# Optimization experiments

Hardware: AMD Instinct MI355X
Metric: run time of the kernel (lower is better)

## Reference

```python
import jax, jax.numpy as jnp
import numpy as np

B, H, W, C = 4, 128, 128, 256
SHIFTS_LOCAL = (1, 2, 4, 8)
SHIFTS_GLOBAL = (1, 2)
LN_EPS = 1e-6
BN_EPS = 1e-3
LAYER_SCALE_INIT = 1e-5


def _glorot(key, shape, fan_in, fan_out):
    lim = (6.0 / (fan_in + fan_out)) ** 0.5
    return jax.random.uniform(key, shape, minval=-lim, maxval=lim, dtype=jnp.float32)


def setup_inputs() -> dict:
    key = jax.random.key(0)
    ks = jax.random.split(key, 10)
    x = jax.random.normal(ks[0], (B, H, W, C), jnp.float32)
    ln_gamma = jnp.ones((C,), jnp.float32)
    w_det = _glorot(ks[1], (C, C), C, C)
    dw1 = _glorot(ks[2], (3, 3, 1, C), 9, 9)   # depthwise 3x3, HWIO with I=1
    dw2 = _glorot(ks[3], (3, 3, 1, C), 9, 9)
    bn_gamma = jnp.ones((C,), jnp.float32)
    bn_mean = jax.random.normal(ks[4], (C,), jnp.float32) * 0.1
    bn_var = jax.random.uniform(ks[5], (C,), minval=0.5, maxval=1.5, dtype=jnp.float32)
    n_loc = 2 * len(SHIFTS_LOCAL) * C   # 'full' mode: sym + antisym per shift
    n_glo = 2 * len(SHIFTS_GLOBAL) * C
    w_geo_local = _glorot(ks[6], (n_loc, C), n_loc, C)
    w_geo_global = _glorot(ks[7], (n_glo, C), n_glo, C)
    w_gate = _glorot(ks[8], (2 * C, C), 2 * C, C)
    gamma_ls = jnp.full((C,), LAYER_SCALE_INIT, jnp.float32)
    return {
        "x": x, "ln_gamma": ln_gamma, "w_det": w_det, "dw1": dw1, "dw2": dw2,
        "bn_gamma": bn_gamma, "bn_mean": bn_mean, "bn_var": bn_var,
        "w_geo_local": w_geo_local, "w_geo_global": w_geo_global,
        "w_gate": w_gate, "gamma_ls": gamma_ls,
    }


def _dwconv(x, k):
    # depthwise 3x3 same conv, NHWC, kernel HWIO with I=1, groups=C
    return jax.lax.conv_general_dilated(
        x, k, window_strides=(1, 1), padding='SAME',
        dimension_numbers=('NHWC', 'HWIO', 'NHWC'),
        feature_group_count=x.shape[-1])


def _geo_prod(a, b, shifts, w):
    # sparse rolling geometric product, cli_mode='full': for each channel
    # shift s emit symmetric (inner) and antisymmetric (wedge) parts, then
    # project the concat back to C channels (bias-free Dense).
    feats = []
    for s in shifts:
        b_s = jnp.roll(b, s, axis=-1)
        a_s = jnp.roll(a, s, axis=-1)
        feats.append(a * b_s + a_s * b)   # inner (symmetric)
        feats.append(a * b_s - a_s * b)   # wedge (antisymmetric)
    return jnp.concatenate(feats, axis=-1) @ w


def reference(x, ln_gamma, w_det, dw1, dw2, bn_gamma, bn_mean, bn_var,
              w_geo_local, w_geo_global, w_gate, gamma_ls):
    # LayerNorm, center=False (scale-only, mean still subtracted)
    mu = jnp.mean(x, axis=-1, keepdims=True)
    var = jnp.var(x, axis=-1, keepdims=True)
    x_norm = (x - mu) / jnp.sqrt(var + LN_EPS) * ln_gamma
    # deterministic stream: bias-free Dense
    z_det = x_norm @ w_det
    # context stream: two depthwise convs + scale-only BN (inference) + SiLU
    z_ctx = _dwconv(_dwconv(x_norm, dw1), dw2)
    z_ctx = jax.nn.silu((z_ctx - bn_mean) / jnp.sqrt(bn_var + BN_EPS) * bn_gamma)
    # ctx_mode='diff'
    z_ctx = z_ctx - z_det
    g_feat = _geo_prod(z_det, z_ctx, SHIFTS_LOCAL, w_geo_local)
    # global context branch
    c_glo = jnp.mean(x_norm, axis=(1, 2), keepdims=True) - z_det
    g_feat = g_feat + _geo_prod(z_det, c_glo, SHIFTS_GLOBAL, w_geo_global)
    # bias-free gated geometric residual (drop_path_rate=0 => identity)
    alpha = jax.nn.sigmoid(jnp.concatenate([x_norm, g_feat], axis=-1) @ w_gate)
    h_mix = (jax.nn.silu(x_norm) + alpha * g_feat) * gamma_ls
    return x + h_mix
```

## Files before the change

### kernel.cpp

```cpp
#include <hip/hip_runtime.h>

typedef __attribute__((ext_vector_type(8))) short bf16x8;
typedef __attribute__((ext_vector_type(8))) unsigned short ushort8;
typedef __attribute__((ext_vector_type(4))) unsigned short ushort4v;
typedef __attribute__((ext_vector_type(4))) float f32x4;
typedef __attribute__((ext_vector_type(4))) float float4v;
typedef __attribute__((ext_vector_type(8))) _Float16 f16x8;

__device__ inline unsigned short f2bf(float f){
  unsigned u = __builtin_bit_cast(unsigned, f);
  return (unsigned short)((u + 0x7fffu + ((u>>16)&1u)) >> 16);
}
__device__ inline float bf2f(unsigned short h){
  return __builtin_bit_cast(float, (unsigned)h << 16);
}
__device__ inline unsigned short f2h(float f){
  return __builtin_bit_cast(unsigned short, (_Float16)f);
}
__device__ inline float h2f(unsigned short u){
  return (float)__builtin_bit_cast(_Float16, u);
}

__device__ inline void gll16(const void* g, void* l){
  __builtin_amdgcn_global_load_lds((const __attribute__((address_space(1))) void*)g,
                                   (__attribute__((address_space(3))) void*)l, 16, 0, 0);
}

__global__ __launch_bounds__(256) void k_ln(const float* __restrict__ x,
                                            const float* __restrict__ g,
                                            unsigned short* __restrict__ A3){
  int wid = threadIdx.x >> 6, lane = threadIdx.x & 63;
  int row = blockIdx.x*4 + wid;
  float4v v = *(const float4v*)&x[(size_t)row*256 + lane*4];
  float4v gv = *(const float4v*)&g[lane*4];
  float s  = v[0]+v[1]+v[2]+v[3];
  float s2 = v[0]*v[0]+v[1]*v[1]+v[2]*v[2]+v[3]*v[3];
  #pragma unroll
  for (int m=32; m>=1; m>>=1){ s += __shfl_xor(s, m, 64); s2 += __shfl_xor(s2, m, 64); }
  float mu  = s*(1.f/256.f);
  float var = s2*(1.f/256.f) - mu*mu;
  float rst = rsqrtf(var + 1e-6f);
  ushort4v o;
  #pragma unroll
  for (int e=0;e<4;e++) o[e] = f2bf((v[e]-mu)*rst*gv[e]);
  *(ushort4v*)&A3[(size_t)row*512 + lane*4] = o;
}

__global__ __launch_bounds__(256) void k_cm1(const unsigned short* __restrict__ A3,
                                             float* __restrict__ psum){
  __shared__ float red[8][256];
  int blk = blockIdx.x, t = threadIdx.x;
  int rs = t >> 5, c8 = (t & 31)*8;
  float a[8] = {0,0,0,0,0,0,0,0};
  #pragma unroll
  for (int i=0; i<8; ++i){
    int row = blk*64 + rs + i*8;
    ushort8 v = *(const ushort8*)&A3[(size_t)row*512 + c8];
    #pragma unroll
    for (int e=0;e<8;e++) a[e] += bf2f(v[e]);
  }
  #pragma unroll
  for (int e=0;e<8;e++) red[rs][c8+e] = a[e];
  __syncthreads();
  float s = red[0][t];
  #pragma unroll
  for (int r=1;r<8;r++) s += red[r][t];
  psum[blk*256 + t] = s;
}
__global__ __launch_bounds__(256) void k_cm2(const float* __restrict__ psum,
                                             float* __restrict__ m){
  int b = blockIdx.x, c = threadIdx.x;
  float s = 0.f;
  for (int ch=0; ch<64; ch++) s += psum[(b*64+ch)*256 + c];
  m[b*256 + c] = s*(1.f/16384.f);
}

__global__ __launch_bounds__(256) void k_prep_nt(const float* __restrict__ W,
                                                 unsigned short* __restrict__ WT, int K){
  int idx = blockIdx.x*256 + threadIdx.x;
  int j = idx / K, k = idx - j*K;
  WT[idx] = f2bf(W[(size_t)k*256 + j]);
}

__global__ __launch_bounds__(256) void k_prep_geoT(const float* __restrict__ wl,
                                                   const float* __restrict__ wg,
                                                   unsigned short* __restrict__ WT){
  int idx = blockIdx.x*256 + threadIdx.x;
  int sg = idx >> 16, rem = idx & 65535;
  int j = rem >> 8, k = rem & 255;
  float v;
  if (sg < 8){
    int si = sg >> 1, s = 1 << si;
    bool neg = sg & 1;
    int krow = neg ? ((k + s) & 255) : k;
    float wi = wl[(size_t)((2*si)*256 + krow)*256 + j];
    float ww = wl[(size_t)((2*si+1)*256 + krow)*256 + j];
    v = neg ? (wi - ww) : (wi + ww);
  } else {
    v = -2.f * wg[(size_t)((sg-8)*2*256 + k)*256 + j];
  }
  WT[idx] = f2h(v);
}

__global__ __launch_bounds__(256) void k_prep_weff(const float* __restrict__ wg,
                                                   const float* __restrict__ m,
                                                   unsigned short* __restrict__ WT){
  int b = blockIdx.x >> 8, c = blockIdx.x & 255, j = threadIdx.x;
  float acc = 0.f;
  #pragma unroll
  for (int si=0; si<2; ++si){
    int s = si+1;
    int cm = (c - s) & 255, cp = (c + s) & 255;
    float wi_c  = wg[(size_t)((2*si)*256 + c)*256 + j];
    float ww_c  = wg[(size_t)((2*si+1)*256 + c)*256 + j];
    float wi_cp = wg[(size_t)((2*si)*256 + cp)*256 + j];
    float ww_cp = wg[(size_t)((2*si+1)*256 + cp)*256 + j];
    acc += m[b*256+cm]*(wi_c+ww_c) + m[b*256+cp]*(wi_cp-ww_cp);
  }
  WT[(size_t)b*65536 + (size_t)j*256 + c] = f2h(acc);
}

__global__ __launch_bounds__(256) void k_prep_wgg(const float* __restrict__ wg,
                                                  unsigned short* __restrict__ WT){
  int idx = blockIdx.x*256 + threadIdx.x;
  int e = idx&7, n=(idx>>3)&255, q=(idx>>11)&3, k32=idx>>13;
  int k = k32*32 + q*8 + e;
  WT[idx] = f2h(wg[(size_t)(256+k)*256 + n]);
}

__global__ __launch_bounds__(256) void k_dwf(const unsigned short* __restrict__ A3,
                                             const float* __restrict__ w1g,
                                             const float* __restrict__ w2g,
                                             const float* __restrict__ bg,
                                             const float* __restrict__ bm_,
                                             const float* __restrict__ bv,
                                             const unsigned short* __restrict__ zdet,
                                             unsigned short* __restrict__ zcx){
  __shared__ unsigned short t0[12800];
  __shared__ unsigned short t1[10368];
  int t = blockIdx.x;
  int img = t >> 6, ty = (t>>3)&7, tx = t&7;
  int c0 = blockIdx.y*32;
  int tid = threadIdx.x;
  int ch = tid & 31;
  int c = c0 + ch;
  for (int v = tid; v < 3200; v += 256){
    int py = v / 160, rem = v - py*160;
    int px = rem >> 3, ch4 = (rem & 7)*4;
    int gpy = ty*16 - 2 + py, gpx = tx*16 - 2 + px;
    ushort4v val = {0,0,0,0};
    if ((unsigned)gpy < 128u && (unsigned)gpx < 128u){
      size_t gp = (size_t)(img*16384 + gpy*128 + gpx);
      val = *(const ushort4v*)&A3[gp*512 + c0 + ch4];
    }
    *(ushort4v*)&t0[(py*20+px)*32 + ch4] = val;
  }
  float w1[9], w2[9];
  #pragma unroll
  for (int k=0;k<9;k++){ w1[k] = w1g[k*256 + c]; w2[k] = w2g[k*256 + c]; }
  __syncthreads();
  for (int p = tid>>5; p < 324; p += 8){
    int py = p / 18, px = p - py*18;
    int gpy = ty*16 - 1 + py, gpx = tx*16 - 1 + px;
    float acc = 0.f;
    #pragma unroll
    for (int dy=0; dy<3; ++dy)
      #pragma unroll
      for (int dx=0; dx<3; ++dx)
        acc += bf2f(t0[((py+dy)*20 + px+dx)*32 + ch]) * w1[dy*3+dx];
    bool valid = ((unsigned)gpy < 128u) && ((unsigned)gpx < 128u);
    t1[p*32 + ch] = valid ? f2h(acc) : (unsigned short)0;
  }
  __syncthreads();
  float bmv = bm_[c];
  float rsbg = rsqrtf(bv[c] + 1e-3f) * bg[c];
  for (int p = tid>>5; p < 256; p += 8){
    int py = p >> 4, px = p & 15;
    float acc = 0.f;
    #pragma unroll
    for (int dy=0; dy<3; ++dy)
      #pragma unroll
      for (int dx=0; dx<3; ++dx)
        acc += h2f(t1[((py+dy)*18 + px+dx)*32 + ch]) * w2[dy*3+dx];
    float tv = (acc - bmv) * rsbg;
    float sv = tv / (1.f + __expf(-tv));
    size_t gp = (size_t)(img*16384 + (ty*16+py)*128 + tx*16+px);
    float z = sv - h2f(zdet[gp*256 + c]);
    zcx[gp*256 + c] = f2h(z);
  }
}

__global__ __launch_bounds__(256) void k_gemmD(const unsigned short* __restrict__ A,
                                               const unsigned short* __restrict__ Bt1,
                                               const unsigned short* __restrict__ Bt2,
                                               unsigned short* __restrict__ o1,
                                               unsigned short* __restrict__ o2){
  __shared__ unsigned short As[128*64];
  __shared__ unsigned short Bss[128*64];
  const int tid=threadIdx.x, lane=tid&63, wid=tid>>6;
  const int nb = blockIdx.x;
  const int bm = blockIdx.y*128;
  const unsigned short* Bt = (nb<2)? Bt1 : Bt2;
  unsigned short* outh = (nb<2)? o1 : o2;
  const int bn = (nb&1)*128;
  const int wr = wid>>1, wc = wid&1;
  f32x4 acc[4][4] = {};
  const int srow = lane>>3;
  const int skc  = ((lane&7) ^ srow) * 8;
  for (int t=0; t<4; ++t){
    int k0 = t*64;
    #pragma unroll
    for (int i=0;i<4;i++){
      int q = wid*4 + i;
      int row = q*8 + srow;
      gll16(A  + (size_t)(bm+row)*512 + k0 + skc, &As[q*512]);
      gll16(Bt + (size_t)(bn+row)*256 + k0 + skc, &Bss[q*512]);
    }
    __syncthreads();
    #pragma unroll
    for (int kk=0; kk<2; ++kk){
      bf16x8 af[4], bfr[4];
      #pragma unroll
      for (int i=0;i<4;i++){
        int rl = wr*64 + i*16 + (lane&15);
        int kc = (kk*32 + (lane>>4)*8) ^ ((rl&7)*8);
        af[i]  = *(const bf16x8*)&As[rl*64 + kc];
        int cl = wc*64 + i*16 + (lane&15);
        int kcb = (kk*32 + (lane>>4)*8) ^ ((cl&7)*8);
        bfr[i] = *(const bf16x8*)&Bss[cl*64 + kcb];
      }
      #pragma unroll
      for (int i=0;i<4;i++)
        #pragma unroll
        for (int j=0;j<4;j++)
          acc[i][j] = __builtin_amdgcn_mfma_f32_16x16x32_bf16(af[i], bfr[j], acc[i][j], 0,0,0);
    }
    __syncthreads();
  }
  #pragma unroll
  for (int i=0;i<4;i++)
    #pragma unroll
    for (int j=0;j<4;j++)
      #pragma unroll
      for (int r=0;r<4;r++){
        int row = bm + wr*64 + i*16 + (lane>>4)*4 + r;
        int col = bn + wc*64 + j*16 + (lane&15);
        outh[(size_t)row*256 + col] = f2h(acc[i][j][r]);
      }
}

template<int S>
__device__ __attribute__((always_inline)) ushort8 shsel(ushort8 hi, ushort8 lo){
  ushort8 r;
  if constexpr (S==0) return hi;
  #pragma unroll
  for (int e=0;e<8;e++) r[e] = (e<S) ? lo[8-S+e] : hi[e-S];
  return r;
}

template<int SEG>
__device__ __attribute__((always_inline)) f16x8 gen2(ushort8 zdh, ushort8 zdl,
      ushort8 zch, ushort8 zcl, ushort8 zcu){
  if constexpr (SEG==10) return __builtin_bit_cast(f16x8, zdh);
  ushort8 sel;
  if constexpr      (SEG==0) sel = shsel<1>(zch, zcl);
  else if constexpr (SEG==1) sel = shsel<7>(zcu, zch);
  else if constexpr (SEG==2) sel = shsel<2>(zch, zcl);
  else if constexpr (SEG==3) sel = shsel<6>(zcu, zch);
  else if constexpr (SEG==4) sel = shsel<4>(zch, zcl);
  else if constexpr (SEG==5) sel = shsel<4>(zcu, zch);
  else if constexpr (SEG==6) sel = zcl;
  else if constexpr (SEG==7) sel = zcu;
  else if constexpr (SEG==8) sel = shsel<1>(zdh, zdl);
  else                       sel = shsel<2>(zdh, zdl);
  return __builtin_bit_cast(f16x8, zdh) * __builtin_bit_cast(f16x8, sel);
}

__global__ __launch_bounds__(256) void k_geo(const unsigned short* __restrict__ zd,
                                             const unsigned short* __restrict__ zc,
                                             const unsigned short* __restrict__ WT_all,
                                             const unsigned short* __restrict__ WeffT,
                                             const unsigned short* __restrict__ WGGP,
                                             const unsigned short* __restrict__ GXB,
                                             const unsigned short* __restrict__ A3,
                                             const float* __restrict__ x,
                                             const float* __restrict__ gls,
                                             float* __restrict__ out){
  __shared__ unsigned short Bs[3][8192];
  const int tid = threadIdx.x, lane = tid&63, wid = tid>>6;
  const int bm = blockIdx.x*64;
  const int img = blockIdx.x >> 8;
  const int wr = wid>>1, wc = wid&1;
  f32x4 acc0[8] = {}, acc1[8] = {};

  const int s4 = tid & 3;
  int inv[4];
  #pragma unroll
  for (int g=0; g<4; ++g){
    int n = g*64 + (tid>>2);
    int sw = (n + (n>>2)) & 3;
    inv[g] = n*256 + ((s4^sw)<<3);
  }
  int roff[8];
  #pragma unroll
  for (int fj=0; fj<8; ++fj){
    int n = wc*128 + fj*16 + (lane&15);
    int sw = (n + (n>>2)) & 3;
    roff[fj] = n*32 + (((lane>>4) ^ sw) << 3);
  }

  const int m0 = bm + wr*32 + (lane&15);
  const unsigned short* zdr0 = zd + (size_t)m0*256;
  const unsigned short* zdr1 = zdr0 + 16*256;
  const unsigned short* zcr0 = zc + (size_t)m0*256;
  const unsigned short* zcr1 = zcr0 + 16*256;

  ushort8 zdh0,zdl0,zch0,zcl0,zcu0, zdh1,zdl1,zch1,zcl1,zcu1;
  int cur = 0;

#define STAGE(BUF, SP, KK) { \
    const unsigned short* Wb = ((SP)<10) ? (WT_all + (SP)*65536) : (WeffT + (size_t)img*65536); \
    const unsigned short* Wk = Wb + (KK)*32; \
    gll16(Wk + inv[0], &Bs[BUF][0*2048 + wid*512]); \
    gll16(Wk + inv[1], &Bs[BUF][1*2048 + wid*512]); \
    gll16(Wk + inv[2], &Bs[BUF][2*2048 + wid*512]); \
    gll16(Wk + inv[3], &Bs[BUF][3*2048 + wid*512]); \
  }

  STAGE(0, 0, 0);
  STAGE(1, 1, 0);

#define STEP(P) { \
    asm volatile("s_waitcnt vmcnt(4)" ::: "memory"); \
    __builtin_amdgcn_s_barrier(); \
    if constexpr ((P)==0){ \
      int kc = k32*32 + (lane>>4)*8; \
      int kl = (kc-8)&255, ku = (kc+8)&255; \
      zdh0 = *(const ushort8*)(zdr0 + kc); zdl0 = *(const ushort8*)(zdr0 + kl); \
      zch0 = *(const ushort8*)(zcr0 + kc); zcl0 = *(const ushort8*)(zcr0 + kl); \
      zcu0 = *(const ushort8*)(zcr0 + ku); \
      zdh1 = *(const ushort8*)(zdr1 + kc); zdl1 = *(const ushort8*)(zdr1 + kl); \
      zch1 = *(const ushort8*)(zcr1 + kc); zcl1 = *(const ushort8*)(zcr1 + kl); \
      zcu1 = *(const ushort8*)(zcr1 + ku); \
    } \
    __builtin_amdgcn_sched_barrier(0); \
    { constexpr int s2 = ((P)+2 <= 10) ? (P)+2 : (P)+2-11; \
      int k2 = k32 + (((P)+2 > 10) ? 1 : 0); if (k2 > 7) k2 = 7; \
      int nbuf = cur+2; if (nbuf >= 3) nbuf -= 3; \
      STAGE(nbuf, s2, k2); } \
    __builtin_amdgcn_sched_barrier(0); \
    f16x8 af0 = gen2<(P)>(zdh0,zdl0,zch0,zcl0,zcu0); \
    f16x8 af1 = gen2<(P)>(zdh1,zdl1,zch1,zcl1,zcu1); \
    const unsigned short* bp = &Bs[cur][0]; \
    __builtin_amdgcn_s_setprio(1); \
    _Pragma("unroll") \
    for (int fj=0; fj<8; ++fj){ \
      f16x8 bfr = *(const f16x8*)&bp[roff[fj]]; \
      acc0[fj] = __builtin_amdgcn_mfma_f32_16x16x32_f16(af0, bfr, acc0[fj], 0,0,0); \
      acc1[fj] = __builtin_amdgcn_mfma_f32_16x16x32_f16(af1, bfr, acc1[fj], 0,0,0); \
    } \
    __builtin_amdgcn_s_setprio(0); \
    cur = cur+1; if (cur >= 3) cur -= 3; \
  }

  for (int k32=0; k32<8; ++k32){
    STEP(0) STEP(1) STEP(2) STEP(3) STEP(4) STEP(5)
    STEP(6) STEP(7) STEP(8) STEP(9) STEP(10)
  }
#undef STEP
#undef STAGE

  asm volatile("s_waitcnt vmcnt(0)" ::: "memory");
  __syncthreads();
  unsigned short* Gs = &Bs[0][0];

  #pragma unroll
  for (int fj=0; fj<8; ++fj)
    #pragma unroll
    for (int r=0; r<4; ++r){
      int col = wc*128 + fj*16 + (lane&15);
      int rl0 = wr*32 + (lane>>4)*4 + r;
      int rl1 = rl0 + 16;
      Gs[rl0*256 + (col ^ ((rl0&7)<<3))] = f2h(acc0[fj][r]);
      Gs[rl1*256 + (col ^ ((rl1&7)<<3))] = f2h(acc1[fj][r]);
    }
  {
    f32x4 zz = {};
    #pragma unroll
    for (int fj=0; fj<8; ++fj){ acc0[fj] = zz; acc1[fj] = zz; }
  }
  __syncthreads();

  const int q = lane>>4;
  #pragma unroll
  for (int k32=0; k32<8; ++k32){
    int kc = k32*32 + q*8;
    int ra0 = wr*32 + (lane&15);
    int ra1 = ra0 + 16;
    f16x8 af0 = *(const f16x8*)&Gs[ra0*256 + (kc ^ ((ra0&7)<<3))];
    f16x8 af1 = *(const f16x8*)&Gs[ra1*256 + (kc ^ ((ra1&7)<<3))];
    const unsigned short* wp = WGGP + k32*8192 + q*2048 + (wc*128 + (lane&15))*8;
    #pragma unroll
    for (int fj=0; fj<8; ++fj){
      f16x8 bfr = *(const f16x8*)(wp + fj*128);
      acc0[fj] = __builtin_amdgcn_mfma_f32_16x16x32_f16(af0, bfr, acc0[fj], 0,0,0);
      acc1[fj] = __builtin_amdgcn_mfma_f32_16x16x32_f16(af1, bfr, acc1[fj], 0,0,0);
    }
  }

  #pragma unroll
  for (int fj=0; fj<8; ++fj)
    #pragma unroll
    for (int r=0; r<4; ++r){
      int col = wc*128 + fj*16 + (lane&15);
      float gm = gls[col];
      #pragma unroll
      for (int g2=0; g2<2; ++g2){
        int rl = wr*32 + (lane>>4)*4 + r + g2*16;
        int row = bm + rl;
        float gf = h2f(Gs[rl*256 + (col ^ ((rl&7)<<3))]);
        float gv = (g2 ? acc1[fj][r] : acc0[fj][r]) + h2f(GXB[(size_t)row*256 + col]);
        float alpha = 1.f/(1.f+__expf(-gv));
        float xn = bf2f(A3[(size_t)row*512 + col]);
        float sl = xn/(1.f+__expf(-xn));
        out[(size_t)row*256 + col] = x[(size_t)row*256 + col] + (sl + alpha*gf)*gm;
      }
    }
}

extern "C" void kernel_launch(void* const* d_in, const int* in_sizes, int n_in,
                              void* d_out, int out_size, void* d_ws, size_t ws_size,
                              hipStream_t stream){
  (void)in_sizes; (void)n_in; (void)out_size; (void)ws_size;
  const float* x    = (const float*)d_in[0];
  const float* lng  = (const float*)d_in[1];
  const float* wdet = (const float*)d_in[2];
  const float* dw1  = (const float*)d_in[3];
  const float* dw2  = (const float*)d_in[4];
  const float* bng  = (const float*)d_in[5];
  const float* bnm  = (const float*)d_in[6];
  const float* bnv  = (const float*)d_in[7];
  const float* wloc = (const float*)d_in[8];
  const float* wglo = (const float*)d_in[9];
  const float* wgat = (const float*)d_in[10];
  const float* gls  = (const float*)d_in[11];
  float* out = (float*)d_out;
  char* ws = (char*)d_ws;

  unsigned short* A3     = (unsigned short*)(ws);
  unsigned short* ZDET   = (unsigned short*)(ws + 67108864);
  unsigned short* GXB    = (unsigned short*)(ws + 100663296);
  unsigned short* ZCX    = (unsigned short*)(ws + 134217728);
  unsigned short* WTALL  = (unsigned short*)(ws + 167772160);
  unsigned short* WEFFT  = (unsigned short*)(ws + 169213952);
  unsigned short* WDETT  = (unsigned short*)(ws + 169738240);
  unsigned short* WGXT   = (unsigned short*)(ws + 169869312);
  unsigned short* WGGP   = (unsigned short*)(ws + 170000384);
  float* PSUM  = (float*)(ws + 170131456);
  float* MMEAN = (float*)(ws + 170393600);

  k_ln<<<16384, 256, 0, stream>>>(x, lng, A3);
  k_cm1<<<256, 256, 0, stream>>>(A3, PSUM);
  k_cm2<<<4, 256, 0, stream>>>(PSUM, MMEAN);
  k_prep_nt<<<256, 256, 0, stream>>>(wdet, WDETT, 256);
  k_prep_nt<<<256, 256, 0, stream>>>(wgat, WGXT, 256);
  k_prep_wgg<<<256, 256, 0, stream>>>(wgat, WGGP);
  k_prep_geoT<<<2560, 256, 0, stream>>>(wloc, wglo, WTALL);
  k_prep_weff<<<1024, 256, 0, stream>>>(wglo, MMEAN, WEFFT);
  k_gemmD<<<dim3(4,512), 256, 0, stream>>>(A3, WDETT, WGXT, ZDET, GXB);
  k_dwf<<<dim3(256,8), 256, 0, stream>>>(A3, dw1, dw2, bng, bnm, bnv, ZDET, ZCX);
  k_geo<<<1024, 256, 0, stream>>>(ZDET, ZCX, WTALL, WEFFT, WGGP, GXB, A3, x, gls, out);
}
```

Before: 337.7 us.

## Fuse x_norm gate GEMM into geo epilogue and drop GXB intermediate

The x_norm half of the gate projection (x_norm @ w_gate[:C]) moves out of the upfront GEMM and into the geo kernel's final gate GEMM. There the x_norm tile is staged into shared memory and accumulated with bf16 MFMAs alongside the existing f16 g_feat MFMAs. This removes writing and re-reading the GXB intermediate (32MB), halves the first GEMM's work, and compacts the x_norm buffer from a 512 to a 256 stride. In exchange, the geo kernel uses more shared memory (64KB) and does twice the MFMA work in its epilogue, which may reduce occupancy.

```diff
diff --git a/kernel.cpp b/kernel.cpp
--- a/kernel.cpp
+++ b/kernel.cpp
@@ -28,7 +28,7 @@
 
 __global__ __launch_bounds__(256) void k_ln(const float* __restrict__ x,
                                             const float* __restrict__ g,
-                                            unsigned short* __restrict__ A3){
+                                            unsigned short* __restrict__ XN){
   int wid = threadIdx.x >> 6, lane = threadIdx.x & 63;
   int row = blockIdx.x*4 + wid;
   float4v v = *(const float4v*)&x[(size_t)row*256 + lane*4];
@@ -43,10 +43,10 @@
   ushort4v o;
   #pragma unroll
   for (int e=0;e<4;e++) o[e] = f2bf((v[e]-mu)*rst*gv[e]);
-  *(ushort4v*)&A3[(size_t)row*512 + lane*4] = o;
-}
-
-__global__ __launch_bounds__(256) void k_cm1(const unsigned short* __restrict__ A3,
+  *(ushort4v*)&XN[(size_t)row*256 + lane*4] = o;
+}
+
+__global__ __launch_bounds__(256) void k_cm1(const unsigned short* __restrict__ XN,
                                              float* __restrict__ psum){
   __shared__ float red[8][256];
   int blk = blockIdx.x, t = threadIdx.x;
@@ -55,7 +55,7 @@
   #pragma unroll
   for (int i=0; i<8; ++i){
     int row = blk*64 + rs + i*8;
-    ushort8 v = *(const ushort8*)&A3[(size_t)row*512 + c8];
+    ushort8 v = *(const ushort8*)&XN[(size_t)row*256 + c8];
     #pragma unroll
     for (int e=0;e<8;e++) a[e] += bf2f(v[e]);
   }
@@ -120,6 +120,13 @@
   WT[(size_t)b*65536 + (size_t)j*256 + c] = f2h(acc);
 }
 
+__global__ __launch_bounds__(256) void k_prep_wgx(const float* __restrict__ wg,
+                                                  unsigned short* __restrict__ WT){
+  int idx = blockIdx.x*256 + threadIdx.x;
+  int e = idx&7, n=(idx>>3)&255, q=(idx>>11)&3, k32=idx>>13;
+  int k = k32*32 + q*8 + e;
+  WT[idx] = f2bf(wg[(size_t)k*256 + n]);
+}
 __global__ __launch_bounds__(256) void k_prep_wgg(const float* __restrict__ wg,
                                                   unsigned short* __restrict__ WT){
   int idx = blockIdx.x*256 + threadIdx.x;
@@ -128,7 +135,7 @@
   WT[idx] = f2h(wg[(size_t)(256+k)*256 + n]);
 }
 
-__global__ __launch_bounds__(256) void k_dwf(const unsigned short* __restrict__ A3,
+__global__ __launch_bounds__(256) void k_dwf(const unsigned short* __restrict__ XN,
                                              const float* __restrict__ w1g,
                                              const float* __restrict__ w2g,
                                              const float* __restrict__ bg,
@@ -151,7 +158,7 @@
     ushort4v val = {0,0,0,0};
     if ((unsigned)gpy < 128u && (unsigned)gpx < 128u){
       size_t gp = (size_t)(img*16384 + gpy*128 + gpx);
-      val = *(const ushort4v*)&A3[gp*512 + c0 + ch4];
+      val = *(const ushort4v*)&XN[gp*256 + c0 + ch4];
     }
     *(ushort4v*)&t0[(py*20+px)*32 + ch4] = val;
   }
@@ -190,19 +197,13 @@
   }
 }
 
-__global__ __launch_bounds__(256) void k_gemmD(const unsigned short* __restrict__ A,
-                                               const unsigned short* __restrict__ Bt1,
-                                               const unsigned short* __restrict__ Bt2,
-                                               unsigned short* __restrict__ o1,
-                                               unsigned short* __restrict__ o2){
+__global__ __launch_bounds__(256) void k_gemm0(const unsigned short* __restrict__ A,
+                                               const unsigned short* __restrict__ Bt,
+                                               unsigned short* __restrict__ outh){
   __shared__ unsigned short As[128*64];
   __shared__ unsigned short Bss[128*64];
   const int tid=threadIdx.x, lane=tid&63, wid=tid>>6;
-  const int nb = blockIdx.x;
-  const int bm = blockIdx.y*128;
-  const unsigned short* Bt = (nb<2)? Bt1 : Bt2;
-  unsigned short* outh = (nb<2)? o1 : o2;
-  const int bn = (nb&1)*128;
+  const int bm = blockIdx.x*128, bn = blockIdx.y*128;
   const int wr = wid>>1, wc = wid&1;
   f32x4 acc[4][4] = {};
   const int srow = lane>>3;
@@ -213,7 +214,7 @@
     for (int i=0;i<4;i++){
       int q = wid*4 + i;
       int row = q*8 + srow;
-      gll16(A  + (size_t)(bm+row)*512 + k0 + skc, &As[q*512]);
+      gll16(A  + (size_t)(bm+row)*256 + k0 + skc, &As[q*512]);
       gll16(Bt + (size_t)(bn+row)*256 + k0 + skc, &Bss[q*512]);
     }
     __syncthreads();
@@ -280,13 +281,13 @@
                                              const unsigned short* __restrict__ zc,
                                              const unsigned short* __restrict__ WT_all,
                                              const unsigned short* __restrict__ WeffT,
+                                             const unsigned short* __restrict__ WGXP,
                                              const unsigned short* __restrict__ WGGP,
-                                             const unsigned short* __restrict__ GXB,
-                                             const unsigned short* __restrict__ A3,
+                                             const unsigned short* __restrict__ XN,
                                              const float* __restrict__ x,
                                              const float* __restrict__ gls,
                                              float* __restrict__ out){
-  __shared__ unsigned short Bs[3][8192];
+  __shared__ unsigned short S[32768];
   const int tid = threadIdx.x, lane = tid&63, wid = tid>>6;
   const int bm = blockIdx.x*64;
   const int img = blockIdx.x >> 8;
@@ -321,10 +322,11 @@
 #define STAGE(BUF, SP, KK) { \
     const unsigned short* Wb = ((SP)<10) ? (WT_all + (SP)*65536) : (WeffT + (size_t)img*65536); \
     const unsigned short* Wk = Wb + (KK)*32; \
-    gll16(Wk + inv[0], &Bs[BUF][0*2048 + wid*512]); \
-    gll16(Wk + inv[1], &Bs[BUF][1*2048 + wid*512]); \
-    gll16(Wk + inv[2], &Bs[BUF][2*2048 + wid*512]); \
-    gll16(Wk + inv[3], &Bs[BUF][3*2048 + wid*512]); \
+    unsigned short* db = S + (BUF)*8192 + wid*512; \
+    gll16(Wk + inv[0], db); \
+    gll16(Wk + inv[1], db + 2048); \
+    gll16(Wk + inv[2], db + 4096); \
+    gll16(Wk + inv[3], db + 6144); \
   }
 
   STAGE(0, 0, 0);
@@ -351,7 +353,7 @@
     __builtin_amdgcn_sched_barrier(0); \
     f16x8 af0 = gen2<(P)>(zdh0,zdl0,zch0,zcl0,zcu0); \
     f16x8 af1 = gen2<(P)>(zdh1,zdl1,zch1,zcl1,zcu1); \
-    const unsigned short* bp = &Bs[cur][0]; \
+    const unsigned short* bp = S + cur*8192; \
     __builtin_amdgcn_s_setprio(1); \
     _Pragma("unroll") \
     for (int fj=0; fj<8; ++fj){ \
@@ -372,7 +374,8 @@
 
   asm volatile("s_waitcnt vmcnt(0)" ::: "memory");
   __syncthreads();
-  unsigned short* Gs = &Bs[0][0];
+  unsigned short* XnS = &S[0];
+  unsigned short* GfS = &S[16384];
 
   #pragma unroll
   for (int fj=0; fj<8; ++fj)
@@ -381,9 +384,18 @@
       int col = wc*128 + fj*16 + (lane&15);
       int rl0 = wr*32 + (lane>>4)*4 + r;
       int rl1 = rl0 + 16;
-      Gs[rl0*256 + (col ^ ((rl0&7)<<3))] = f2h(acc0[fj][r]);
-      Gs[rl1*256 + (col ^ ((rl1&7)<<3))] = f2h(acc1[fj][r]);
+      GfS[rl0*256 + (col ^ ((rl0&7)<<3))] = f2h(acc0[fj][r]);
+      GfS[rl1*256 + (col ^ ((rl1&7)<<3))] = f2h(acc1[fj][r]);
     }
+  #pragma unroll
+  for (int i=0; i<8; ++i){
+    int group = wid*8 + i;
+    int chunk0 = group*64;
+    int row = (chunk0 + lane) >> 5;
+    int c3  = (chunk0 + lane) & 31;
+    const unsigned short* src = XN + (size_t)(bm + row)*256 + ((c3 ^ (row&7))<<3);
+    gll16(src, XnS + chunk0*8);
+  }
   {
     f32x4 zz = {};
     #pragma unroll
@@ -392,40 +404,47 @@
   __syncthreads();
 
   const int q = lane>>4;
+  const int ra0 = wr*32 + (lane&15);
+  const int ra1 = ra0 + 16;
   #pragma unroll
   for (int k32=0; k32<8; ++k32){
     int kc = k32*32 + q*8;
-    int ra0 = wr*32 + (lane&15);
-    int ra1 = ra0 + 16;
-    f16x8 af0 = *(const f16x8*)&Gs[ra0*256 + (kc ^ ((ra0&7)<<3))];
-    f16x8 af1 = *(const f16x8*)&Gs[ra1*256 + (kc ^ ((ra1&7)<<3))];
-    const unsigned short* wp = WGGP + k32*8192 + q*2048 + (wc*128 + (lane&15))*8;
+    int chx = (k32*4 + q);
+    bf16x8 ax0 = *(const bf16x8*)&XnS[ra0*256 + ((chx ^ (ra0&7))<<3)];
+    bf16x8 ax1 = *(const bf16x8*)&XnS[ra1*256 + ((chx ^ (ra1&7))<<3)];
+    f16x8 ag0 = *(const f16x8*)&GfS[ra0*256 + (kc ^ ((ra0&7)<<3))];
+    f16x8 ag1 = *(const f16x8*)&GfS[ra1*256 + (kc ^ ((ra1&7)<<3))];
+    const unsigned short* wpx = WGXP + k32*8192 + q*2048 + (wc*128 + (lane&15))*8;
+    const unsigned short* wpg = WGGP + k32*8192 + q*2048 + (wc*128 + (lane&15))*8;
     #pragma unroll
     for (int fj=0; fj<8; ++fj){
-      f16x8 bfr = *(const f16x8*)(wp + fj*128);
-      acc0[fj] = __builtin_amdgcn_mfma_f32_16x16x32_f16(af0, bfr, acc0[fj], 0,0,0);
-      acc1[fj] = __builtin_amdgcn_mfma_f32_16x16x32_f16(af1, bfr, acc1[fj], 0,0,0);
+      bf16x8 bx = *(const bf16x8*)(wpx + fj*128);
+      acc0[fj] = __builtin_amdgcn_mfma_f32_16x16x32_bf16(ax0, bx, acc0[fj], 0,0,0);
+      acc1[fj] = __builtin_amdgcn_mfma_f32_16x16x32_bf16(ax1, bx, acc1[fj], 0,0,0);
+      f16x8 bg = *(const f16x8*)(wpg + fj*128);
+      acc0[fj] = __builtin_amdgcn_mfma_f32_16x16x32_f16(ag0, bg, acc0[fj], 0,0,0);
+      acc1[fj] = __builtin_amdgcn_mfma_f32_16x16x32_f16(ag1, bg, acc1[fj], 0,0,0);
     }
   }
 
   #pragma unroll
-  for (int fj=0; fj<8; ++fj)
-    #pragma unroll
-    for (int r=0; r<4; ++r){
-      int col = wc*128 + fj*16 + (lane&15);
-      float gm = gls[col];
+  for (int fj=0; fj<8; ++fj){
+    int col = wc*128 + fj*16 + (lane&15);
+    float gm = gls[col];
+    #pragma unroll
+    for (int r=0; r<4; ++r)
       #pragma unroll
       for (int g2=0; g2<2; ++g2){
         int rl = wr*32 + (lane>>4)*4 + r + g2*16;
         int row = bm + rl;
-        float gf = h2f(Gs[rl*256 + (col ^ ((rl&7)<<3))]);
-        float gv = (g2 ? acc1[fj][r] : acc0[fj][r]) + h2f(GXB[(size_t)row*256 + col]);
+        float gf = h2f(GfS[rl*256 + (col ^ ((rl&7)<<3))]);
+        float xn = bf2f(XnS[rl*256 + (((col>>3) ^ (rl&7))<<3) + (col&7)]);
+        float gv = g2 ? acc1[fj][r] : acc0[fj][r];
         float alpha = 1.f/(1.f+__expf(-gv));
-        float xn = bf2f(A3[(size_t)row*512 + col]);
         float sl = xn/(1.f+__expf(-xn));
         out[(size_t)row*256 + col] = x[(size_t)row*256 + col] + (sl + alpha*gf)*gm;
       }
-    }
+  }
 }
 
 extern "C" void kernel_launch(void* const* d_in, const int* in_sizes, int n_in,
@@ -447,27 +466,26 @@
   float* out = (float*)d_out;
   char* ws = (char*)d_ws;
 
-  unsigned short* A3     = (unsigned short*)(ws);
-  unsigned short* ZDET   = (unsigned short*)(ws + 67108864);
-  unsigned short* GXB    = (unsigned short*)(ws + 100663296);
-  unsigned short* ZCX    = (unsigned short*)(ws + 134217728);
-  unsigned short* WTALL  = (unsigned short*)(ws + 167772160);
-  unsigned short* WEFFT  = (unsigned short*)(ws + 169213952);
-  unsigned short* WDETT  = (unsigned short*)(ws + 169738240);
-  unsigned short* WGXT   = (unsigned short*)(ws + 169869312);
-  unsigned short* WGGP   = (unsigned short*)(ws + 170000384);
-  float* PSUM  = (float*)(ws + 170131456);
-  float* MMEAN = (float*)(ws + 170393600);
-
-  k_ln<<<16384, 256, 0, stream>>>(x, lng, A3);
-  k_cm1<<<256, 256, 0, stream>>>(A3, PSUM);
+  unsigned short* XN    = (unsigned short*)(ws);
+  unsigned short* ZDET  = (unsigned short*)(ws + 33554432);
+  unsigned short* ZCX   = (unsigned short*)(ws + 67108864);
+  unsigned short* WTALL = (unsigned short*)(ws + 100663296);
+  unsigned short* WEFFT = (unsigned short*)(ws + 101974016);
+  unsigned short* WDETT = (unsigned short*)(ws + 102498304);
+  unsigned short* WGXP  = (unsigned short*)(ws + 102629376);
+  unsigned short* WGGP  = (unsigned short*)(ws + 102760448);
+  float* PSUM  = (float*)(ws + 102891520);
+  float* MMEAN = (float*)(ws + 103153664);
+
+  k_ln<<<16384, 256, 0, stream>>>(x, lng, XN);
+  k_cm1<<<256, 256, 0, stream>>>(XN, PSUM);
   k_cm2<<<4, 256, 0, stream>>>(PSUM, MMEAN);
   k_prep_nt<<<256, 256, 0, stream>>>(wdet, WDETT, 256);
-  k_prep_nt<<<256, 256, 0, stream>>>(wgat, WGXT, 256);
+  k_prep_wgx<<<256, 256, 0, stream>>>(wgat, WGXP);
   k_prep_wgg<<<256, 256, 0, stream>>>(wgat, WGGP);
   k_prep_geoT<<<2560, 256, 0, stream>>>(wloc, wglo, WTALL);
   k_prep_weff<<<1024, 256, 0, stream>>>(wglo, MMEAN, WEFFT);
-  k_gemmD<<<dim3(4,512), 256, 0, stream>>>(A3, WDETT, WGXT, ZDET, GXB);
-  k_dwf<<<dim3(256,8), 256, 0, stream>>>(A3, dw1, dw2, bng, bnm, bnv, ZDET, ZCX);
-  k_geo<<<1024, 256, 0, stream>>>(ZDET, ZCX, WTALL, WEFFT, WGGP, GXB, A3, x, gls, out);
-}
+  k_gemm0<<<dim3(512,2), 256, 0, stream>>>(XN, WDETT, ZDET);
+  k_dwf<<<dim3(256,8), 256, 0, stream>>>(XN, dw1, dw2, bng, bnm, bnv, ZDET, ZCX);
+  k_geo<<<1024, 256, 0, stream>>>(ZDET, ZCX, WTALL, WEFFT, WGXP, WGGP, XN, x, gls, out);
+}
```

After: 404.8 us. 19.9% more time.
